# Kernel tuning notes

Measured on AMD Instinct MI355X. Metric: run time of the kernel, lower is better.

Reference implementation:

```python
import jax, jax.numpy as jnp
import numpy as np

N, H, D, G = 8192, 512, 256, 64
TAU, LAM, ALPHA, BETA = 0.5, 0.5, 1.0, 1.0
EPS_G, EPS_L = 1e-6, 1e-5


def setup_inputs() -> dict:
    key = jax.random.key(0)
    ks = jax.random.split(key, 8)
    za = jax.random.normal(ks[0], (N, H), dtype=jnp.float32)
    zb = jax.random.normal(ks[1], (N, H), dtype=jnp.float32)
    pos = jax.random.uniform(ks[2], (N, N), dtype=jnp.float32)
    batch = (jnp.arange(N, dtype=jnp.int32) * G) // N  # sorted, covers all G groups
    s_h = np.sqrt(2.0 / H).astype(np.float32)  # kaiming fan_in relu
    W1 = jax.random.normal(ks[3], (H, H), dtype=jnp.float32) * s_h
    b1 = jnp.zeros((H,), dtype=jnp.float32)
    W2 = jax.random.normal(ks[4], (H, H), dtype=jnp.float32) * s_h
    b2 = jnp.zeros((H,), dtype=jnp.float32)
    W3 = jax.random.normal(ks[5], (H, D), dtype=jnp.float32) * s_h
    b3 = jnp.zeros((D,), dtype=jnp.float32)
    a1 = jnp.full((1,), 0.5, dtype=jnp.float32)
    g1 = jnp.ones((H,), dtype=jnp.float32)
    be1 = jnp.zeros((H,), dtype=jnp.float32)
    a2 = jnp.full((1,), 0.5, dtype=jnp.float32)
    g2 = jnp.ones((H,), dtype=jnp.float32)
    be2 = jnp.zeros((H,), dtype=jnp.float32)
    return {"za": za, "zb": zb, "pos": pos, "batch": batch,
            "W1": W1, "b1": b1, "a1": a1, "g1": g1, "be1": be1,
            "W2": W2, "b2": b2, "a2": a2, "g2": g2, "be2": be2,
            "W3": W3, "b3": b3}


def _project(z, W1, b1, a1, g1, be1, W2, b2, a2, g2, be2, W3, b3):
    h = z @ W1 + b1
    h = jnp.tanh(a1 * h) * g1 + be1  # DyT
    h = h @ W2 + b2
    h = jnp.tanh(a2 * h) * g2 + be2  # DyT
    p = h @ W3 + b3
    return p * jax.nn.sigmoid(p)  # z1_proj * sigmoid(z1_proj)


def reference(za, zb, pos, batch, W1, b1, a1, g1, be1, W2, b2, a2, g2, be2, W3, b3):
    za_p = _project(za, W1, b1, a1, g1, be1, W2, b2, a2, g2, be2, W3, b3)
    zb_p = _project(zb, W1, b1, a1, g1, be1, W2, b2, a2, g2, be2, W3, b3)

    # exp(cosine / tau): same matrix used by global_contrast (sim) and local_contrast
    na = jnp.linalg.norm(za_p, axis=-1, keepdims=True)  # [N,1]
    nb = jnp.linalg.norm(zb_p, axis=-1, keepdims=True)  # [N,1]
    m = jnp.exp((za_p @ zb_p.T) / (na * nb.T) / TAU)    # [N,N]

    # global contrast
    a2b = m / (jnp.sum(m, axis=1, keepdims=True) + EPS_G)
    lori_a = -jnp.mean(jnp.log(jnp.sum(a2b * pos, axis=-1)))
    b2a = m.T
    b2a = b2a / (jnp.sum(b2a, axis=1, keepdims=True) + EPS_G)
    lori_b = -jnp.mean(jnp.log(jnp.sum(b2a * pos, axis=-1)))
    global_loss = LAM * lori_a + (1.0 - LAM) * lori_b

    # local contrast: per-group sums via one-hot matmul (replaces O(G^2) mask loop)
    pos_sim = jnp.diagonal(m)                              # [N]
    pos_sim_graph = jax.ops.segment_sum(pos_sim, batch, num_segments=G)  # [G]
    hot = jax.nn.one_hot(batch, G, dtype=m.dtype)          # [N,G]
    batch_sim = hot.T @ m @ hot                            # [G,G]
    graph_sim = jnp.diagonal(batch_sim)
    neg0 = jnp.sum(batch_sim, axis=0) - graph_sim
    neg1 = jnp.sum(batch_sim, axis=1) - graph_sim
    loss0 = jnp.mean(jnp.log(pos_sim_graph / (neg0 + EPS_L)))
    loss1 = jnp.mean(jnp.log(pos_sim_graph / (neg1 + EPS_L)))
    inter_loss = (loss0 + loss1) / 2.0
    inner_loss = -jnp.mean(jnp.log(pos_sim_graph / (graph_sim - pos_sim_graph + EPS_L)))
    local_loss = ALPHA * inter_loss + BETA * inner_loss

    total_loss = global_loss + local_loss
    return total_loss, jnp.concatenate((za_p, zb_p), axis=1)
```

## Files before the change

### kernel.cpp

```cpp
#include <hip/hip_runtime.h>
#include <hip/hip_bf16.h>
#include <cstdint>
#include <cstddef>


typedef __bf16 bf16;
typedef __bf16 bf16x4 __attribute__((ext_vector_type(4)));
typedef __bf16 bf16x8 __attribute__((ext_vector_type(8)));
typedef float  f32x4  __attribute__((ext_vector_type(4)));

#define NROWS 8192
#define HDIM  512
#define DDIM  256
#define GGRP  64
#define INV_TAU 2.0f

__device__ __forceinline__ void async_ld16(const void* g, void* l) {
    __builtin_amdgcn_global_load_lds(
        (__attribute__((address_space(1))) void*)(g),
        (__attribute__((address_space(3))) void*)(l), 16, 0, 0);
}

__device__ __forceinline__ void mfma_tile_128(
    const bf16* __restrict__ A, const bf16* __restrict__ Bt, int K,
    int row0, int col0, bf16* ldsA, bf16* ldsB, f32x4 acc[4][4])
{
    const int tid  = threadIdx.x;
    const int lane = tid & 63;
    const int wave = tid >> 6;
    const int wrow = (wave >> 1) * 64;
    const int wcol = (wave & 1) * 64;
    const int lrow = lane & 15;
    const int lk8  = (lane >> 4) * 8;

#pragma unroll
    for (int i = 0; i < 4; i++)
#pragma unroll
        for (int j = 0; j < 4; j++) acc[i][j] = (f32x4){0.f, 0.f, 0.f, 0.f};

    for (int k0 = 0; k0 < K; k0 += 32) {
#pragma unroll
        for (int t = 0; t < 2; t++) {
            int f = t * 256 + tid;
            int r = f >> 2;
            int c = (f & 3) * 8;
            async_ld16(A  + (size_t)(row0 + r) * K + k0 + c,
                       ldsA + (size_t)(t * 256 + wave * 64) * 8);
            async_ld16(Bt + (size_t)(col0 + r) * K + k0 + c,
                       ldsB + (size_t)(t * 256 + wave * 64) * 8);
        }
        __syncthreads();

        bf16x8 af[4], bfr[4];
#pragma unroll
        for (int fi = 0; fi < 4; fi++)
            af[fi] = *(const bf16x8*)(ldsA + (wrow + fi * 16 + lrow) * 32 + lk8);
#pragma unroll
        for (int fj = 0; fj < 4; fj++)
            bfr[fj] = *(const bf16x8*)(ldsB + (wcol + fj * 16 + lrow) * 32 + lk8);
#pragma unroll
        for (int fi = 0; fi < 4; fi++)
#pragma unroll
            for (int fj = 0; fj < 4; fj++)
                acc[fi][fj] = __builtin_amdgcn_mfma_f32_16x16x32_bf16(
                    af[fi], bfr[fj], acc[fi][fj], 0, 0, 0);
        __syncthreads();
    }
}

__global__ __launch_bounds__(256) void gemm_dyt(
    const bf16* __restrict__ A, const bf16* __restrict__ Bt, bf16* __restrict__ C,
    int K, int N,
    const float* __restrict__ bias, const float* __restrict__ alph,
    const float* __restrict__ gam, const float* __restrict__ bet)
{
    __shared__ __align__(16) bf16 ldsA[128 * 32];
    __shared__ __align__(16) bf16 ldsB[128 * 32];
    f32x4 acc[4][4];
    const int row0 = blockIdx.y * 128, col0 = blockIdx.x * 128;
    mfma_tile_128(A, Bt, K, row0, col0, ldsA, ldsB, acc);

    const int lane = threadIdx.x & 63, wave = threadIdx.x >> 6;
    const int wrow = (wave >> 1) * 64, wcol = (wave & 1) * 64;
    const int lcol = lane & 15, lrg = (lane >> 4) * 4;
    const float a = alph[0];
#pragma unroll
    for (int fi = 0; fi < 4; fi++) {
        const int rbase = row0 + wrow + fi * 16 + lrg;
#pragma unroll
        for (int fj = 0; fj < 4; fj++) {
            const int cg = col0 + wcol + fj * 16 + lcol;
            const float bcol = bias[cg], gcol = gam[cg], becol = bet[cg];
#pragma unroll
            for (int r = 0; r < 4; r++) {
                float x = acc[fi][fj][r] + bcol;
                float y = tanhf(a * x) * gcol + becol;
                C[(size_t)(rbase + r) * N + cg] = (bf16)y;
            }
        }
    }
}

__global__ __launch_bounds__(256) void gemm_silu(
    const bf16* __restrict__ A, const bf16* __restrict__ Bt,
    bf16* __restrict__ P16, float* __restrict__ out1, float* __restrict__ n2,
    const float* __restrict__ bias)
{
    __shared__ __align__(16) bf16 ldsA[128 * 32];
    __shared__ __align__(16) bf16 ldsB[128 * 32];
    f32x4 acc[4][4];
    const int row0 = blockIdx.y * 128, col0 = blockIdx.x * 128;
    mfma_tile_128(A, Bt, 512, row0, col0, ldsA, ldsB, acc);

    const int lane = threadIdx.x & 63, wave = threadIdx.x >> 6;
    const int wrow = (wave >> 1) * 64, wcol = (wave & 1) * 64;
    const int lcol = lane & 15, lrg = (lane >> 4) * 4;

    float nacc[4][4];
#pragma unroll
    for (int i = 0; i < 4; i++)
#pragma unroll
        for (int r = 0; r < 4; r++) nacc[i][r] = 0.f;

#pragma unroll
    for (int fi = 0; fi < 4; fi++) {
        const int rbase = row0 + wrow + fi * 16 + lrg;
#pragma unroll
        for (int fj = 0; fj < 4; fj++) {
            const int cg = col0 + wcol + fj * 16 + lcol;
            const float bcol = bias[cg];
#pragma unroll
            for (int r = 0; r < 4; r++) {
                const int rg = rbase + r;
                float x = acc[fi][fj][r] + bcol;
                float y = x / (1.f + __expf(-x));
                P16[(size_t)rg * 256 + cg] = (bf16)y;
                size_t oidx = (rg < NROWS) ? ((size_t)rg * 512 + cg)
                                           : ((size_t)(rg - NROWS) * 512 + 256 + cg);
                out1[oidx] = y;
                nacc[fi][r] += y * y;
            }
        }
    }
#pragma unroll
    for (int fi = 0; fi < 4; fi++)
#pragma unroll
        for (int r = 0; r < 4; r++) {
            float v = nacc[fi][r];
            v += __shfl_xor(v, 1); v += __shfl_xor(v, 2);
            v += __shfl_xor(v, 4); v += __shfl_xor(v, 8);
            if (lcol == 0)
                atomicAdd(&n2[row0 + wrow + fi * 16 + lrg + r], v);
        }
}

template <int PASS1>
__global__ __launch_bounds__(256) void sim_kernel(
    const bf16* __restrict__ PA, const bf16* __restrict__ PB,
    const float* __restrict__ rnA, const float* __restrict__ rnB,
    const float* __restrict__ pos,
    float* __restrict__ rsum, float* __restrict__ wsum,
    float* __restrict__ bsim, float* __restrict__ psg)
{
    __shared__ __align__(16) bf16 ldsA[128 * 32];
    __shared__ __align__(16) bf16 ldsB[128 * 32];
    f32x4 acc[4][4];
    const int I = blockIdx.y, J = blockIdx.x;
    const int row0 = I * 128, col0 = J * 128;
    mfma_tile_128(PA, PB, 256, row0, col0, ldsA, ldsB, acc);

    const int lane = threadIdx.x & 63, wave = threadIdx.x >> 6;
    const int wrow = (wave >> 1) * 64, wcol = (wave & 1) * 64;
    const int lcol = lane & 15, lrg = (lane >> 4) * 4;

    float racc[4][4], sacc[4][4];
#pragma unroll
    for (int i = 0; i < 4; i++)
#pragma unroll
        for (int r = 0; r < 4; r++) { racc[i][r] = 0.f; sacc[i][r] = 0.f; }
    float msum = 0.f;

#pragma unroll
    for (int fi = 0; fi < 4; fi++) {
        const int rbase = row0 + wrow + fi * 16 + lrg;
        float rna[4];
#pragma unroll
        for (int r = 0; r < 4; r++) rna[r] = rnA[rbase + r] * INV_TAU;
#pragma unroll
        for (int fj = 0; fj < 4; fj++) {
            const int cg = col0 + wcol + fj * 16 + lcol;
            const float rnb = rnB[cg];
#pragma unroll
            for (int r = 0; r < 4; r++) {
                float mval = __expf(acc[fi][fj][r] * rna[r] * rnb);
                float pv = pos[(size_t)(rbase + r) * NROWS + cg];
                racc[fi][r] += mval;
                sacc[fi][r] += mval * pv;
                if (PASS1) {
                    msum += mval;
                    if (I == J && (rbase + r) == cg)
                        atomicAdd(&psg[I], mval);
                }
            }
        }
    }
#pragma unroll
    for (int fi = 0; fi < 4; fi++)
#pragma unroll
        for (int r = 0; r < 4; r++) {
            float rv = racc[fi][r], sv = sacc[fi][r];
            rv += __shfl_xor(rv, 1); rv += __shfl_xor(rv, 2);
            rv += __shfl_xor(rv, 4); rv += __shfl_xor(rv, 8);
            sv += __shfl_xor(sv, 1); sv += __shfl_xor(sv, 2);
            sv += __shfl_xor(sv, 4); sv += __shfl_xor(sv, 8);
            if (lcol == 0) {
                const int rg = row0 + wrow + fi * 16 + lrg + r;
                atomicAdd(&rsum[rg], rv);
                atomicAdd(&wsum[rg], sv);
            }
        }
    if (PASS1) {
        msum += __shfl_xor(msum, 1);  msum += __shfl_xor(msum, 2);
        msum += __shfl_xor(msum, 4);  msum += __shfl_xor(msum, 8);
        msum += __shfl_xor(msum, 16); msum += __shfl_xor(msum, 32);
        if (lane == 0) atomicAdd(&bsim[I * GGRP + J], msum);
    }
}

__global__ void cast4_kernel(const float4* __restrict__ x, bf16x4* __restrict__ y, int n4)
{
    int i = blockIdx.x * blockDim.x + threadIdx.x;
    if (i < n4) {
        float4 v = x[i];
        bf16x4 o;
        o[0] = (bf16)v.x; o[1] = (bf16)v.y; o[2] = (bf16)v.z; o[3] = (bf16)v.w;
        y[i] = o;
    }
}

__global__ void transpose_cast(const float* __restrict__ W, bf16* __restrict__ Wt,
                               int R, int C)
{
    __shared__ float tile[32][33];
    const int c0 = blockIdx.x * 32, r0 = blockIdx.y * 32;
    const int tx = threadIdx.x, ty = threadIdx.y;
    for (int i = ty; i < 32; i += 8)
        tile[i][tx] = W[(size_t)(r0 + i) * C + c0 + tx];
    __syncthreads();
    for (int i = ty; i < 32; i += 8)
        Wt[(size_t)(c0 + i) * R + r0 + tx] = (bf16)tile[tx][i];
}

__global__ void rsqrt_kernel(const float* __restrict__ x, float* __restrict__ y, int n)
{
    int i = blockIdx.x * blockDim.x + threadIdx.x;
    if (i < n) y[i] = rsqrtf(fmaxf(x[i], 1e-30f));
}

__global__ void loss_kernel(
    const float* __restrict__ rowsum, const float* __restrict__ colsum,
    const float* __restrict__ sa, const float* __restrict__ sb,
    const float* __restrict__ bs, const float* __restrict__ psg,
    float* __restrict__ out)
{
    __shared__ float red[8];
    const int tid = threadIdx.x;
    float la = 0.f, lb = 0.f;
    for (int i = tid; i < NROWS; i += 256) {
        la += __logf(sa[i] / (rowsum[i] + 1e-6f));
        lb += __logf(sb[i] / (colsum[i] + 1e-6f));
    }
    for (int m = 1; m < 64; m <<= 1) {
        la += __shfl_xor(la, m);
        lb += __shfl_xor(lb, m);
    }
    if ((tid & 63) == 0) { red[tid >> 6] = la; red[4 + (tid >> 6)] = lb; }
    __syncthreads();

    float l0 = 0.f, l1 = 0.f, lin = 0.f;
    if (tid < GGRP) {
        const float d = bs[tid * GGRP + tid];
        float c0 = 0.f, c1 = 0.f;
        for (int a = 0; a < GGRP; a++) { c0 += bs[a * GGRP + tid]; c1 += bs[tid * GGRP + a]; }
        const float p = psg[tid];
        l0  = __logf(p / (c0 - d + 1e-5f));
        l1  = __logf(p / (c1 - d + 1e-5f));
        lin = __logf(p / (d - p + 1e-5f));
    }
    for (int m = 1; m < 64; m <<= 1) {
        l0 += __shfl_xor(l0, m); l1 += __shfl_xor(l1, m); lin += __shfl_xor(lin, m);
    }
    if (tid == 0) {
        const float lat = red[0] + red[1] + red[2] + red[3];
        const float lbt = red[4] + red[5] + red[6] + red[7];
        const float lori_a = -lat / (float)NROWS;
        const float lori_b = -lbt / (float)NROWS;
        const float global_loss = 0.5f * (lori_a + lori_b);
        const float inter = 0.5f * (l0 + l1) / (float)GGRP;
        const float inner = -lin / (float)GGRP;
        out[0] = global_loss + inter + inner;
    }
}

extern "C" void kernel_launch(void* const* d_in, const int* in_sizes, int n_in,
                              void* d_out, int out_size, void* d_ws, size_t ws_size,
                              hipStream_t stream)
{
    const float* za  = (const float*)d_in[0];
    const float* zb  = (const float*)d_in[1];
    const float* pos = (const float*)d_in[2];
    const float* W1  = (const float*)d_in[4];
    const float* b1  = (const float*)d_in[5];
    const float* a1  = (const float*)d_in[6];
    const float* g1  = (const float*)d_in[7];
    const float* be1 = (const float*)d_in[8];
    const float* W2  = (const float*)d_in[9];
    const float* b2  = (const float*)d_in[10];
    const float* a2  = (const float*)d_in[11];
    const float* g2  = (const float*)d_in[12];
    const float* be2 = (const float*)d_in[13];
    const float* W3  = (const float*)d_in[14];
    const float* b3  = (const float*)d_in[15];
    float* out = (float*)d_out;

    char* ws = (char*)d_ws;
    float* rowsum = (float*)(ws);
    float* colsum = rowsum + 8192;
    float* s_a    = colsum + 8192;
    float* s_b    = s_a + 8192;
    float* n2     = s_b + 8192;
    float* bsim   = n2 + 16384;
    float* psg    = bsim + 4096;
    const size_t accum_bytes = (size_t)(8192 * 4 + 16384 + 4096 + 64) * 4;

    float* rn  = (float*)(ws + 213248);
    bf16* Z16  = (bf16*)(ws + 213248 + 65536);
    bf16* h1   = Z16 + (size_t)16384 * 512;
    bf16* p16  = h1 + (size_t)16384 * 512;
    bf16* W1t  = p16 + (size_t)16384 * 256;
    bf16* W2t  = W1t + (size_t)512 * 512;
    bf16* W3t  = W2t + (size_t)512 * 512;

    hipMemsetAsync(d_ws, 0, accum_bytes, stream);

    const int n4 = NROWS * HDIM / 4;
    cast4_kernel<<<n4 / 256, 256, 0, stream>>>((const float4*)za, (bf16x4*)Z16, n4);
    cast4_kernel<<<n4 / 256, 256, 0, stream>>>((const float4*)zb,
                                               (bf16x4*)(Z16 + (size_t)NROWS * HDIM), n4);
    dim3 tb(32, 8);
    transpose_cast<<<dim3(16, 16), tb, 0, stream>>>(W1, W1t, 512, 512);
    transpose_cast<<<dim3(16, 16), tb, 0, stream>>>(W2, W2t, 512, 512);
    transpose_cast<<<dim3(8, 16),  tb, 0, stream>>>(W3, W3t, 512, 256);

    gemm_dyt<<<dim3(4, 128), 256, 0, stream>>>(Z16, W1t, h1, 512, 512, b1, a1, g1, be1);
    gemm_dyt<<<dim3(4, 128), 256, 0, stream>>>(h1, W2t, Z16 , 512, 512, b2, a2, g2, be2);
    gemm_silu<<<dim3(2, 128), 256, 0, stream>>>(Z16, W3t, p16, out + 1, n2, b3);
    rsqrt_kernel<<<16384 / 256, 256, 0, stream>>>(n2, rn, 16384);

    const bf16* pa = p16;
    const bf16* pb = p16 + (size_t)NROWS * DDIM;
    sim_kernel<1><<<dim3(64, 64), 256, 0, stream>>>(pa, pb, rn, rn + NROWS, pos,
                                                    rowsum, s_a, bsim, psg);
    sim_kernel<0><<<dim3(64, 64), 256, 0, stream>>>(pb, pa, rn + NROWS, rn, pos,
                                                    colsum, s_b, nullptr, nullptr);

    loss_kernel<<<1, 256, 0, stream>>>(rowsum, colsum, s_a, s_b, bsim, psg, out);
}
```

Before: 819.8 us.

## Prefetch pos tile into LDS asynchronously and reduce diagonal atomics per wave

```diff
diff --git a/kernel.cpp b/kernel.cpp
--- a/kernel.cpp
+++ b/kernel.cpp
@@ -162,14 +162,29 @@
     float* __restrict__ rsum, float* __restrict__ wsum,
     float* __restrict__ bsim, float* __restrict__ psg)
 {
-    __shared__ __align__(16) bf16 ldsA[128 * 32];
-    __shared__ __align__(16) bf16 ldsB[128 * 32];
+    __shared__ __align__(16) bf16  ldsA[128 * 32];
+    __shared__ __align__(16) bf16  ldsB[128 * 32];
+    __shared__ __align__(16) float ldsP[128 * 128];
     f32x4 acc[4][4];
     const int I = blockIdx.y, J = blockIdx.x;
     const int row0 = I * 128, col0 = J * 128;
+
+    const int tid  = threadIdx.x;
+    const int lane = tid & 63, wave = tid >> 6;
+
+#pragma unroll
+    for (int t = 0; t < 16; t++) {
+        const int cid = t * 4 + wave;
+        const int f4  = cid * 64 + lane;
+        const int r   = f4 >> 5;
+        const int cgs = f4 & 31;
+        const int cgp = cgs ^ (r & 4);
+        async_ld16(pos + (size_t)(row0 + r) * NROWS + col0 + cgp * 4,
+                   ldsP + (size_t)cid * 256);
+    }
+
     mfma_tile_128(PA, PB, 256, row0, col0, ldsA, ldsB, acc);
 
-    const int lane = threadIdx.x & 63, wave = threadIdx.x >> 6;
     const int wrow = (wave >> 1) * 64, wcol = (wave & 1) * 64;
     const int lcol = lane & 15, lrg = (lane >> 4) * 4;
 
@@ -179,27 +194,30 @@
 #pragma unroll
         for (int r = 0; r < 4; r++) { racc[i][r] = 0.f; sacc[i][r] = 0.f; }
     float msum = 0.f;
+    float dacc = 0.f;
 
 #pragma unroll
     for (int fi = 0; fi < 4; fi++) {
-        const int rbase = row0 + wrow + fi * 16 + lrg;
+        const int lrow0 = wrow + fi * 16 + lrg;
+        const int rbase = row0 + lrow0;
         float rna[4];
 #pragma unroll
         for (int r = 0; r < 4; r++) rna[r] = rnA[rbase + r] * INV_TAU;
 #pragma unroll
         for (int fj = 0; fj < 4; fj++) {
-            const int cg = col0 + wcol + fj * 16 + lcol;
+            const int lc = wcol + fj * 16 + lcol;
+            const int cg = col0 + lc;
             const float rnb = rnB[cg];
 #pragma unroll
             for (int r = 0; r < 4; r++) {
                 float mval = __expf(acc[fi][fj][r] * rna[r] * rnb);
-                float pv = pos[(size_t)(rbase + r) * NROWS + cg];
+                const int lr = lrow0 + r;
+                float pv = ldsP[lr * 128 + (lc ^ ((lr & 4) << 2))];
                 racc[fi][r] += mval;
                 sacc[fi][r] += mval * pv;
                 if (PASS1) {
                     msum += mval;
-                    if (I == J && (rbase + r) == cg)
-                        atomicAdd(&psg[I], mval);
+                    if (I == J && lr == lc) dacc += mval;
                 }
             }
         }
@@ -224,6 +242,12 @@
         msum += __shfl_xor(msum, 4);  msum += __shfl_xor(msum, 8);
         msum += __shfl_xor(msum, 16); msum += __shfl_xor(msum, 32);
         if (lane == 0) atomicAdd(&bsim[I * GGRP + J], msum);
+        if (I == J) {
+            dacc += __shfl_xor(dacc, 1);  dacc += __shfl_xor(dacc, 2);
+            dacc += __shfl_xor(dacc, 4);  dacc += __shfl_xor(dacc, 8);
+            dacc += __shfl_xor(dacc, 16); dacc += __shfl_xor(dacc, 32);
+            if (lane == 0) atomicAdd(&psg[I], dacc);
+        }
     }
 }
 
```

After: 932.6 us. 13.8% more time.

## Fuse row and column similarity passes into one symmetric-pair tile kernel

Applied to the files above, without the earlier changes.

```diff
diff --git a/kernel.cpp b/kernel.cpp
--- a/kernel.cpp
+++ b/kernel.cpp
@@ -2,6 +2,7 @@
 #include <hip/hip_bf16.h>
 #include <cstdint>
 #include <cstddef>
+#include <cmath>
 
 
 typedef __bf16 bf16;
@@ -154,76 +155,181 @@
         }
 }
 
-template <int PASS1>
-__global__ __launch_bounds__(256) void sim_kernel(
-    const bf16* __restrict__ PA, const bf16* __restrict__ PB,
+__device__ __forceinline__ void prefetch_pos(
+    const float* __restrict__ pos, int pr0, int pc0, float* ldsP)
+{
+    const int tid = threadIdx.x, wave = tid >> 6;
+#pragma unroll
+    for (int t = 0; t < 4; t++) {
+        const int f4 = t * 256 + tid;
+        const int r  = f4 >> 4;
+        const int gd = f4 & 15;
+        const int gs = gd ^ (r & 15);
+        async_ld16(pos + (size_t)(pr0 + r) * NROWS + pc0 + gs * 4,
+                   ldsP + (size_t)(t * 256 + wave * 64) * 4);
+    }
+}
+
+__device__ __forceinline__ void mfma_tile_64(
+    const bf16* __restrict__ A, const bf16* __restrict__ Bt,
+    int arow0, int brow0, bf16* ldsA, bf16* ldsB, f32x4 acc[2][2])
+{
+    const int tid  = threadIdx.x;
+    const int lane = tid & 63;
+    const int wave = tid >> 6;
+    const int wrow = (wave >> 1) * 32;
+    const int wcol = (wave & 1) * 32;
+    const int lrow = lane & 15;
+    const int lk8  = (lane >> 4) * 8;
+    const int sr   = tid >> 2;
+    const int sc   = (tid & 3) * 8;
+
+#pragma unroll
+    for (int i = 0; i < 2; i++)
+#pragma unroll
+        for (int j = 0; j < 2; j++) acc[i][j] = (f32x4){0.f, 0.f, 0.f, 0.f};
+
+    for (int k0 = 0; k0 < 256; k0 += 32) {
+        async_ld16(A  + (size_t)(arow0 + sr) * DDIM + k0 + sc, ldsA + wave * 64 * 8);
+        async_ld16(Bt + (size_t)(brow0 + sr) * DDIM + k0 + sc, ldsB + wave * 64 * 8);
+        __syncthreads();
+
+        bf16x8 af[2], bfr[2];
+#pragma unroll
+        for (int fi = 0; fi < 2; fi++)
+            af[fi] = *(const bf16x8*)(ldsA + (wrow + fi * 16 + lrow) * 32 + lk8);
+#pragma unroll
+        for (int fj = 0; fj < 2; fj++)
+            bfr[fj] = *(const bf16x8*)(ldsB + (wcol + fj * 16 + lrow) * 32 + lk8);
+#pragma unroll
+        for (int fi = 0; fi < 2; fi++)
+#pragma unroll
+            for (int fj = 0; fj < 2; fj++)
+                acc[fi][fj] = __builtin_amdgcn_mfma_f32_16x16x32_bf16(
+                    af[fi], bfr[fj], acc[fi][fj], 0, 0, 0);
+        __syncthreads();
+    }
+}
+
+__device__ __forceinline__ void sim_epilogue(
+    const f32x4 acc[2][2], const float* Pa, const float* Pb,
     const float* __restrict__ rnA, const float* __restrict__ rnB,
-    const float* __restrict__ pos,
-    float* __restrict__ rsum, float* __restrict__ wsum,
-    float* __restrict__ bsim, float* __restrict__ psg)
-{
-    __shared__ __align__(16) bf16 ldsA[128 * 32];
-    __shared__ __align__(16) bf16 ldsB[128 * 32];
-    f32x4 acc[4][4];
-    const int I = blockIdx.y, J = blockIdx.x;
-    const int row0 = I * 128, col0 = J * 128;
-    mfma_tile_128(PA, PB, 256, row0, col0, ldsA, ldsB, acc);
-
+    int u, int v, bool do_diag,
+    float* rowsum, float* colsum, float* sa, float* sb,
+    float* bsim, float* psg)
+{
     const int lane = threadIdx.x & 63, wave = threadIdx.x >> 6;
-    const int wrow = (wave >> 1) * 64, wcol = (wave & 1) * 64;
-    const int lcol = lane & 15, lrg = (lane >> 4) * 4;
-
-    float racc[4][4], sacc[4][4];
-#pragma unroll
-    for (int i = 0; i < 4; i++)
-#pragma unroll
-        for (int r = 0; r < 4; r++) { racc[i][r] = 0.f; sacc[i][r] = 0.f; }
+    const int wrow = (wave >> 1) * 32, wcol = (wave & 1) * 32;
+    const int lcol = lane & 15, lrg = lane >> 4;
+
+    float rna[2][4], rnb[2];
+#pragma unroll
+    for (int fi = 0; fi < 2; fi++)
+#pragma unroll
+        for (int r = 0; r < 4; r++)
+            rna[fi][r] = rnA[u * 64 + wrow + fi * 16 + lrg * 4 + r] * INV_TAU;
+#pragma unroll
+    for (int fj = 0; fj < 2; fj++)
+        rnb[fj] = rnB[v * 64 + wcol + fj * 16 + lcol];
+
+    float rowm[2][4], rowp[2][4], colm[2], colp[2];
+#pragma unroll
+    for (int fi = 0; fi < 2; fi++)
+#pragma unroll
+        for (int r = 0; r < 4; r++) { rowm[fi][r] = 0.f; rowp[fi][r] = 0.f; }
+    colm[0] = colm[1] = colp[0] = colp[1] = 0.f;
+    float dacc = 0.f;
+
+#pragma unroll
+    for (int fi = 0; fi < 2; fi++) {
+#pragma unroll
+        for (int fj = 0; fj < 2; fj++) {
+#pragma unroll
+            for (int r = 0; r < 4; r++) {
+                const int la = wrow + fi * 16 + lrg * 4 + r;
+                const int lb = wcol + fj * 16 + lcol;
+                float m = __expf(acc[fi][fj][r] * rna[fi][r] * rnb[fj]);
+                float pa = Pa[(la << 6) + ((((lb >> 2) ^ (la & 15)) << 2) | (lb & 3))];
+                float pb = Pb[(lb << 6) + ((((la >> 2) ^ (lb & 15)) << 2) | (la & 3))];
+                rowm[fi][r] += m;  rowp[fi][r] += m * pa;
+                colm[fj]    += m;  colp[fj]    += m * pb;
+                if (do_diag && la == lb) dacc += m;
+            }
+        }
+    }
+
     float msum = 0.f;
-
-#pragma unroll
-    for (int fi = 0; fi < 4; fi++) {
-        const int rbase = row0 + wrow + fi * 16 + lrg;
-        float rna[4];
-#pragma unroll
-        for (int r = 0; r < 4; r++) rna[r] = rnA[rbase + r] * INV_TAU;
-#pragma unroll
-        for (int fj = 0; fj < 4; fj++) {
-            const int cg = col0 + wcol + fj * 16 + lcol;
-            const float rnb = rnB[cg];
-#pragma unroll
-            for (int r = 0; r < 4; r++) {
-                float mval = __expf(acc[fi][fj][r] * rna[r] * rnb);
-                float pv = pos[(size_t)(rbase + r) * NROWS + cg];
-                racc[fi][r] += mval;
-                sacc[fi][r] += mval * pv;
-                if (PASS1) {
-                    msum += mval;
-                    if (I == J && (rbase + r) == cg)
-                        atomicAdd(&psg[I], mval);
-                }
-            }
-        }
-    }
-#pragma unroll
-    for (int fi = 0; fi < 4; fi++)
+#pragma unroll
+    for (int fi = 0; fi < 2; fi++)
 #pragma unroll
         for (int r = 0; r < 4; r++) {
-            float rv = racc[fi][r], sv = sacc[fi][r];
+            float rv = rowm[fi][r], sv = rowp[fi][r];
+            msum += rv;
             rv += __shfl_xor(rv, 1); rv += __shfl_xor(rv, 2);
             rv += __shfl_xor(rv, 4); rv += __shfl_xor(rv, 8);
             sv += __shfl_xor(sv, 1); sv += __shfl_xor(sv, 2);
             sv += __shfl_xor(sv, 4); sv += __shfl_xor(sv, 8);
             if (lcol == 0) {
-                const int rg = row0 + wrow + fi * 16 + lrg + r;
-                atomicAdd(&rsum[rg], rv);
-                atomicAdd(&wsum[rg], sv);
+                const int rg = u * 64 + wrow + fi * 16 + lrg * 4 + r;
+                atomicAdd(&rowsum[rg], rv);
+                atomicAdd(&sa[rg], sv);
             }
         }
-    if (PASS1) {
-        msum += __shfl_xor(msum, 1);  msum += __shfl_xor(msum, 2);
-        msum += __shfl_xor(msum, 4);  msum += __shfl_xor(msum, 8);
-        msum += __shfl_xor(msum, 16); msum += __shfl_xor(msum, 32);
-        if (lane == 0) atomicAdd(&bsim[I * GGRP + J], msum);
+#pragma unroll
+    for (int fj = 0; fj < 2; fj++) {
+        float cv = colm[fj], sv = colp[fj];
+        cv += __shfl_xor(cv, 16); cv += __shfl_xor(cv, 32);
+        sv += __shfl_xor(sv, 16); sv += __shfl_xor(sv, 32);
+        if (lrg == 0) {
+            const int cg = v * 64 + wcol + fj * 16 + lcol;
+            atomicAdd(&colsum[cg], cv);
+            atomicAdd(&sb[cg], sv);
+        }
+    }
+    msum += __shfl_xor(msum, 1);  msum += __shfl_xor(msum, 2);
+    msum += __shfl_xor(msum, 4);  msum += __shfl_xor(msum, 8);
+    msum += __shfl_xor(msum, 16); msum += __shfl_xor(msum, 32);
+    if (lane == 0) atomicAdd(&bsim[(u >> 1) * GGRP + (v >> 1)], msum);
+    if (do_diag) {
+        dacc += __shfl_xor(dacc, 1);  dacc += __shfl_xor(dacc, 2);
+        dacc += __shfl_xor(dacc, 4);  dacc += __shfl_xor(dacc, 8);
+        dacc += __shfl_xor(dacc, 16); dacc += __shfl_xor(dacc, 32);
+        if (lane == 0) atomicAdd(&psg[u >> 1], dacc);
+    }
+}
+
+__global__ __launch_bounds__(256, 4) void sim_pair(
+    const bf16* __restrict__ PA, const bf16* __restrict__ PB,
+    const float* __restrict__ rnA, const float* __restrict__ rnB,
+    const float* __restrict__ pos,
+    float* __restrict__ rowsum, float* __restrict__ colsum,
+    float* __restrict__ sa, float* __restrict__ sb,
+    float* __restrict__ bsim, float* __restrict__ psg)
+{
+    __shared__ __align__(16) bf16  ldsA[64 * 32];
+    __shared__ __align__(16) bf16  ldsB[64 * 32];
+    __shared__ __align__(16) float ldsP1[64 * 64];
+    __shared__ __align__(16) float ldsP2[64 * 64];
+
+    const int p = blockIdx.x;
+    int I = (int)((257.0 - sqrt(66049.0 - 8.0 * (double)p)) * 0.5);
+    while ((I + 1) * 128 - ((I + 1) * I) / 2 <= p) ++I;
+    while (I * 128 - (I * (I - 1)) / 2 > p) --I;
+    const int J = I + (p - (I * 128 - (I * (I - 1)) / 2));
+    const bool diag = (I == J);
+
+    prefetch_pos(pos, I * 64, J * 64, ldsP1);
+    if (!diag) prefetch_pos(pos, J * 64, I * 64, ldsP2);
+    const float* Pji = diag ? ldsP1 : ldsP2;
+
+    f32x4 acc[2][2];
+    mfma_tile_64(PA, PB, I * 64, J * 64, ldsA, ldsB, acc);
+    sim_epilogue(acc, ldsP1, Pji, rnA, rnB, I, J, diag,
+                 rowsum, colsum, sa, sb, bsim, psg);
+    if (!diag) {
+        mfma_tile_64(PA, PB, J * 64, I * 64, ldsA, ldsB, acc);
+        sim_epilogue(acc, ldsP2, ldsP1, rnA, rnB, J, I, false,
+                     rowsum, colsum, sa, sb, bsim, psg);
     }
 }
 
@@ -359,10 +465,8 @@
 
     const bf16* pa = p16;
     const bf16* pb = p16 + (size_t)NROWS * DDIM;
-    sim_kernel<1><<<dim3(64, 64), 256, 0, stream>>>(pa, pb, rn, rn + NROWS, pos,
-                                                    rowsum, s_a, bsim, psg);
-    sim_kernel<0><<<dim3(64, 64), 256, 0, stream>>>(pb, pa, rn + NROWS, rn, pos,
-                                                    colsum, s_b, nullptr, nullptr);
+    sim_pair<<<dim3(128 * 129 / 2), 256, 0, stream>>>(pa, pb, rn, rn + NROWS, pos,
+                                                      rowsum, colsum, s_a, s_b, bsim, psg);
 
     loss_kernel<<<1, 256, 0, stream>>>(rowsum, colsum, s_a, s_b, bsim, psg, out);
 }
```

Result: faster. 727.9 us (-11.2%).

## Replace tiled sim kernel with flash-style register-resident row streaming over columns

Applied to the files above, without the earlier changes.

```diff
diff --git a/kernel.cpp b/kernel.cpp
--- a/kernel.cpp
+++ b/kernel.cpp
@@ -155,57 +155,106 @@
 }
 
 template <int PASS1>
-__global__ __launch_bounds__(256) void sim_kernel(
+__global__ __launch_bounds__(256, 2) void flash_sim(
     const bf16* __restrict__ PA, const bf16* __restrict__ PB,
     const float* __restrict__ rnA, const float* __restrict__ rnB,
     const float* __restrict__ pos,
     float* __restrict__ rsum, float* __restrict__ wsum,
     float* __restrict__ bsim, float* __restrict__ psg)
 {
-    __shared__ __align__(16) bf16 ldsA[128 * 32];
-    __shared__ __align__(16) bf16 ldsB[128 * 32];
-    f32x4 acc[4][4];
-    const int I = blockIdx.y, J = blockIdx.x;
-    const int row0 = I * 128, col0 = J * 128;
-    mfma_tile_128(PA, PB, 256, row0, col0, ldsA, ldsB, acc);
-
-    const int lane = threadIdx.x & 63, wave = threadIdx.x >> 6;
-    const int wrow = (wave >> 1) * 64, wcol = (wave & 1) * 64;
-    const int lcol = lane & 15, lrg = (lane >> 4) * 4;
-
-    float racc[4][4], sacc[4][4];
-#pragma unroll
-    for (int i = 0; i < 4; i++)
-#pragma unroll
-        for (int r = 0; r < 4; r++) { racc[i][r] = 0.f; sacc[i][r] = 0.f; }
-    float msum = 0.f;
-
-#pragma unroll
-    for (int fi = 0; fi < 4; fi++) {
-        const int rbase = row0 + wrow + fi * 16 + lrg;
-        float rna[4];
-#pragma unroll
-        for (int r = 0; r < 4; r++) rna[r] = rnA[rbase + r] * INV_TAU;
-#pragma unroll
-        for (int fj = 0; fj < 4; fj++) {
-            const int cg = col0 + wcol + fj * 16 + lcol;
-            const float rnb = rnB[cg];
-#pragma unroll
-            for (int r = 0; r < 4; r++) {
-                float mval = __expf(acc[fi][fj][r] * rna[r] * rnb);
-                float pv = pos[(size_t)(rbase + r) * NROWS + cg];
-                racc[fi][r] += mval;
-                sacc[fi][r] += mval * pv;
-                if (PASS1) {
-                    msum += mval;
-                    if (I == J && (rbase + r) == cg)
-                        atomicAdd(&psg[I], mval);
+    const int lane = threadIdx.x & 63;
+    const int wave = threadIdx.x >> 6;
+    const int lrow = lane & 15;
+    const int lk8  = (lane >> 4) * 8;
+    const int lrg  = lane >> 4;
+    const int R0   = blockIdx.y * 128 + wave * 32;
+    const int C0   = blockIdx.x * 1024;
+
+    bf16x8 a[2][8];
+#pragma unroll
+    for (int fi = 0; fi < 2; fi++)
+#pragma unroll
+        for (int kk = 0; kk < 8; kk++)
+            a[fi][kk] = *(const bf16x8*)(
+                PA + (size_t)(R0 + fi * 16 + lrow) * DDIM + kk * 32 + lk8);
+
+    float rna[2][4];
+#pragma unroll
+    for (int fi = 0; fi < 2; fi++)
+#pragma unroll
+        for (int r = 0; r < 4; r++)
+            rna[fi][r] = rnA[R0 + fi * 16 + lrg * 4 + r] * INV_TAU;
+
+    float racc[2][4], sacc[2][4];
+#pragma unroll
+    for (int fi = 0; fi < 2; fi++)
+#pragma unroll
+        for (int r = 0; r < 4; r++) { racc[fi][r] = 0.f; sacc[fi][r] = 0.f; }
+    float msum = 0.f, dacc = 0.f;
+
+#pragma unroll 2
+    for (int ct = 0; ct < 32; ct++) {
+        const int c0 = C0 + ct * 32;
+
+        bf16x8 b[2][8];
+#pragma unroll
+        for (int fj = 0; fj < 2; fj++)
+#pragma unroll
+            for (int kk = 0; kk < 8; kk++)
+                b[fj][kk] = *(const bf16x8*)(
+                    PB + (size_t)(c0 + fj * 16 + lrow) * DDIM + kk * 32 + lk8);
+
+        f32x4 acc[2][2];
+#pragma unroll
+        for (int fi = 0; fi < 2; fi++)
+#pragma unroll
+            for (int fj = 0; fj < 2; fj++) acc[fi][fj] = (f32x4){0.f, 0.f, 0.f, 0.f};
+#pragma unroll
+        for (int kk = 0; kk < 8; kk++)
+#pragma unroll
+            for (int fi = 0; fi < 2; fi++)
+#pragma unroll
+                for (int fj = 0; fj < 2; fj++)
+                    acc[fi][fj] = __builtin_amdgcn_mfma_f32_16x16x32_bf16(
+                        a[fi][kk], b[fj][kk], acc[fi][fj], 0, 0, 0);
+
+        float rnb[2];
+        rnb[0] = rnB[c0 + lrow];
+        rnb[1] = rnB[c0 + 16 + lrow];
+
+        const bool diag_tile = PASS1 && (c0 == R0);
+#pragma unroll
+        for (int fi = 0; fi < 2; fi++)
+#pragma unroll
+            for (int fj = 0; fj < 2; fj++)
+#pragma unroll
+                for (int r = 0; r < 4; r++) {
+                    float m = __expf(acc[fi][fj][r] * rna[fi][r] * rnb[fj]);
+                    float pv = pos[(size_t)(R0 + fi * 16 + lrg * 4 + r) * NROWS
+                                   + c0 + fj * 16 + lrow];
+                    racc[fi][r] += m;
+                    sacc[fi][r] += m * pv;
+                    if (PASS1) {
+                        msum += m;
+                        if (diag_tile &&
+                            (fi * 16 + lrg * 4 + r) == (fj * 16 + lrow))
+                            dacc += m;
+                    }
                 }
-            }
-        }
-    }
-#pragma unroll
-    for (int fi = 0; fi < 4; fi++)
+
+        if (PASS1 && (ct & 3) == 3) {
+            float v = msum;
+            v += __shfl_xor(v, 1);  v += __shfl_xor(v, 2);
+            v += __shfl_xor(v, 4);  v += __shfl_xor(v, 8);
+            v += __shfl_xor(v, 16); v += __shfl_xor(v, 32);
+            if (lane == 0)
+                atomicAdd(&bsim[blockIdx.y * GGRP + (c0 >> 7)], v);
+            msum = 0.f;
+        }
+    }
+
+#pragma unroll
+    for (int fi = 0; fi < 2; fi++)
 #pragma unroll
         for (int r = 0; r < 4; r++) {
             float rv = racc[fi][r], sv = sacc[fi][r];
@@ -213,17 +262,17 @@
             rv += __shfl_xor(rv, 4); rv += __shfl_xor(rv, 8);
             sv += __shfl_xor(sv, 1); sv += __shfl_xor(sv, 2);
             sv += __shfl_xor(sv, 4); sv += __shfl_xor(sv, 8);
-            if (lcol == 0) {
-                const int rg = row0 + wrow + fi * 16 + lrg + r;
+            if (lrow == 0) {
+                const int rg = R0 + fi * 16 + lrg * 4 + r;
                 atomicAdd(&rsum[rg], rv);
                 atomicAdd(&wsum[rg], sv);
             }
         }
-    if (PASS1) {
-        msum += __shfl_xor(msum, 1);  msum += __shfl_xor(msum, 2);
-        msum += __shfl_xor(msum, 4);  msum += __shfl_xor(msum, 8);
-        msum += __shfl_xor(msum, 16); msum += __shfl_xor(msum, 32);
-        if (lane == 0) atomicAdd(&bsim[I * GGRP + J], msum);
+    if (PASS1 && blockIdx.x == (unsigned)(R0 >> 10)) {
+        dacc += __shfl_xor(dacc, 1);  dacc += __shfl_xor(dacc, 2);
+        dacc += __shfl_xor(dacc, 4);  dacc += __shfl_xor(dacc, 8);
+        dacc += __shfl_xor(dacc, 16); dacc += __shfl_xor(dacc, 32);
+        if (lane == 0) atomicAdd(&psg[blockIdx.y], dacc);
     }
 }
 
@@ -359,10 +408,10 @@
 
     const bf16* pa = p16;
     const bf16* pb = p16 + (size_t)NROWS * DDIM;
-    sim_kernel<1><<<dim3(64, 64), 256, 0, stream>>>(pa, pb, rn, rn + NROWS, pos,
-                                                    rowsum, s_a, bsim, psg);
-    sim_kernel<0><<<dim3(64, 64), 256, 0, stream>>>(pb, pa, rn + NROWS, rn, pos,
-                                                    colsum, s_b, nullptr, nullptr);
+    flash_sim<1><<<dim3(8, 64), 256, 0, stream>>>(pa, pb, rn, rn + NROWS, pos,
+                                                  rowsum, s_a, bsim, psg);
+    flash_sim<0><<<dim3(8, 64), 256, 0, stream>>>(pb, pa, rn + NROWS, rn, pos,
+                                                  colsum, s_b, nullptr, nullptr);
 
     loss_kernel<<<1, 256, 0, stream>>>(rowsum, colsum, s_a, s_b, bsim, psg, out);
 }
```

Result: faster. 749.0 us (-8.6%).
